# Optimization experiments

Measured on AMD Instinct MI355X. Metric: run time of the kernel, lower is better.

Reference implementation:

```python
import jax, jax.numpy as jnp
import numpy as np

B, T, C, H, HS = 4, 2048, 384, 6, 64
EPS = 1e-5


def setup_inputs() -> dict:
    key = jax.random.key(0)
    ks = jax.random.split(key, 8)
    s = lambda fan_in: 1.0 / np.sqrt(fan_in)
    return {
        "x": jax.random.normal(ks[0], (B, T, C), jnp.float32),
        "wq": jax.random.normal(ks[1], (H, C, HS), jnp.float32) * s(C),
        "wk": jax.random.normal(ks[2], (H, C, HS), jnp.float32) * s(C),
        "wv": jax.random.normal(ks[3], (H, C, HS), jnp.float32) * s(C),
        "w_proj": jax.random.normal(ks[4], (C, C), jnp.float32) * s(C),
        "b_proj": jnp.zeros((C,), jnp.float32),
        "w1": jax.random.normal(ks[5], (C, 4 * C), jnp.float32) * s(C),
        "b1": jnp.zeros((4 * C,), jnp.float32),
        "w2": jax.random.normal(ks[6], (4 * C, C), jnp.float32) * s(4 * C),
        "b2": jnp.zeros((C,), jnp.float32),
        "g1": jnp.ones((C,), jnp.float32),
        "be1": jnp.zeros((C,), jnp.float32),
        "g2": jnp.ones((C,), jnp.float32),
        "be2": jnp.zeros((C,), jnp.float32),
    }


def _layernorm(z, g, b):
    m = jnp.mean(z, axis=-1, keepdims=True)
    v = jnp.mean((z - m) ** 2, axis=-1, keepdims=True)
    return (z - m) * jax.lax.rsqrt(v + EPS) * g + b


def reference(x, wq, wk, wv, w_proj, b_proj, w1, b1, w2, b2, g1, be1, g2, be2):
    Bx, Tx, Cx = x.shape
    h = _layernorm(x, g1, be1)
    # per-head projections, no bias
    q = jnp.einsum('btc,hcd->bhtd', h, wq)
    k = jnp.einsum('btc,hcd->bhtd', h, wk)
    v = jnp.einsum('btc,hcd->bhtd', h, wv)
    # NOTE: source scales by full embedding dim C, not head_size
    scores = jnp.einsum('bhtd,bhsd->bhts', q, k) * (Cx ** -0.5)
    mask = jnp.tril(jnp.ones((Tx, Tx), bool))  # tril causal mask
    scores = jnp.where(mask[None, None], scores, -jnp.inf)
    # Faithful to source: softmax over dim=1 of (B,T,T) == QUERY axis (axis=2 here)
    w = jax.nn.softmax(scores, axis=2)
    out = jnp.einsum('bhts,bhsd->bhtd', w, v)
    out = out.transpose(0, 2, 1, 3).reshape(Bx, Tx, Cx)  # concat heads
    out = out @ w_proj + b_proj
    x = x + out  # residual 1
    h2 = _layernorm(x, g2, be2)
    f = jax.nn.relu(h2 @ w1 + b1) @ w2 + b2
    return x + f  # residual 2
```

## Files before the change

kernel.cpp:

```cpp
#include <hip/hip_runtime.h>
#include <hip/hip_bf16.h>


#define BB 4
#define TT 2048
#define CC 384
#define HH 6
#define HS 64
#define BT 8192
#define C4 1536
#define VST 2080
#define SCALE 0.05103103630798288f

typedef __attribute__((ext_vector_type(8))) short short8;
typedef __attribute__((ext_vector_type(4))) float f32x4;
typedef __hip_bfloat16 bf16_t;

__device__ inline short8 ld8(const bf16_t* p) { return *reinterpret_cast<const short8*>(p); }
__device__ inline float tof(float v) { return v; }
__device__ inline float tof(bf16_t v) { return __bfloat162float(v); }
#define MFMA(a, b, c) __builtin_amdgcn_mfma_f32_16x16x32_bf16(a, b, c, 0, 0, 0)

__global__ __launch_bounds__(256) void zinit_kernel(float* __restrict__ p, int n4) {
    int i = blockIdx.x * 256 + threadIdx.x;
    if (i < n4) ((f32x4*)p)[i] = (f32x4){0.f, 0.f, 0.f, 0.f};
}

__global__ __launch_bounds__(256) void castbf_kernel(const float* __restrict__ src,
                                                     bf16_t* __restrict__ dst) {
    int i = (blockIdx.x * 256 + threadIdx.x) * 4;
    f32x4 v = *(const f32x4*)(src + i);
#pragma unroll
    for (int j = 0; j < 4; j++) dst[i + j] = __float2bfloat16(v[j]);
}

__device__ inline void tc(const float* __restrict__ src, bf16_t* __restrict__ dst,
                          int R, int Cc, int idx) {
    int rc = R * Cc;
    int b = idx / rc;
    int rem = idx - b * rc;
    int c = rem / R;
    int r = rem - c * R;
    dst[b * rc + c * R + r] = __float2bfloat16(src[b * rc + r * Cc + c]);
}
#define RW  147456
#define RW1 589824
#define NTC (3*RW + RW + 2*RW1)
#define NZ  (BT*CC/4)
__global__ __launch_bounds__(256) void prep_kernel(const float* __restrict__ wq,
                                                   const float* __restrict__ wk,
                                                   const float* __restrict__ wv,
                                                   const float* __restrict__ wproj,
                                                   const float* __restrict__ w1,
                                                   const float* __restrict__ w2,
                                                   bf16_t* __restrict__ wall,
                                                   bf16_t* __restrict__ wpt,
                                                   bf16_t* __restrict__ w1t,
                                                   bf16_t* __restrict__ w2t,
                                                   float* __restrict__ attnf) {
    int i = blockIdx.x * 256 + threadIdx.x;
    if (i < RW)                tc(wq, wall, CC, HS, i);
    else if (i < 2*RW)         tc(wk, wall + RW, CC, HS, i - RW);
    else if (i < 3*RW)         tc(wv, wall + 2*RW, CC, HS, i - 2*RW);
    else if (i < 4*RW)         tc(wproj, wpt, CC, CC, i - 3*RW);
    else if (i < 4*RW + RW1)   tc(w1, w1t, CC, C4, i - 4*RW);
    else if (i < NTC)          tc(w2, w2t, C4, CC, i - 4*RW - RW1);
    else {
        int z = i - NTC;
        if (z < NZ) ((f32x4*)attnf)[z] = (f32x4){0.f, 0.f, 0.f, 0.f};
    }
}

template <typename T>
__global__ __launch_bounds__(256) void ln_kernel(const T* __restrict__ x,
                                                 const float* __restrict__ g,
                                                 const float* __restrict__ be,
                                                 bf16_t* __restrict__ out) {
    int wave = threadIdx.x >> 6, lane = threadIdx.x & 63;
    int row = blockIdx.x * 4 + wave;
    const T* xr = x + (size_t)row * CC;
    float v[6];
    float s = 0.f;
#pragma unroll
    for (int i = 0; i < 6; i++) { v[i] = tof(xr[lane + i * 64]); s += v[i]; }
#pragma unroll
    for (int off = 32; off > 0; off >>= 1) s += __shfl_xor(s, off, 64);
    float mean = s * (1.f / 384.f);
    float s2 = 0.f;
#pragma unroll
    for (int i = 0; i < 6; i++) { float d = v[i] - mean; s2 += d * d; }
#pragma unroll
    for (int off = 32; off > 0; off >>= 1) s2 += __shfl_xor(s2, off, 64);
    float rstd = rsqrtf(s2 * (1.f / 384.f) + 1e-5f);
    bf16_t* orow = out + (size_t)row * CC;
#pragma unroll
    for (int i = 0; i < 6; i++) {
        int c = lane + i * 64;
        orow[c] = __float2bfloat16((v[i] - mean) * rstd * g[c] + be[c]);
    }
}

template <int KDIM, int EPI>
__global__ __launch_bounds__(256) void gemm128_kernel(const bf16_t* __restrict__ A,
                                                      const bf16_t* __restrict__ Bt,
                                                      const float* __restrict__ bias,
                                                      const void* __restrict__ resid,
                                                      void* __restrict__ o0,
                                                      void* __restrict__ o1,
                                                      void* __restrict__ o2, int N) {
    const int m0 = blockIdx.x * 128, n0 = blockIdx.y * 128;
    const int tid = threadIdx.x;
    const int lane = tid & 63, wave = tid >> 6;
    const int r16 = lane & 15, quad = lane >> 4;
    const int wm = (wave >> 1) * 64, wn = (wave & 1) * 64;
    __shared__ bf16_t Ash[128][40];
    __shared__ bf16_t Bsh[128][40];
    f32x4 zero = {0.f, 0.f, 0.f, 0.f};
    f32x4 acc[4][4];
#pragma unroll
    for (int i = 0; i < 4; i++)
#pragma unroll
        for (int j = 0; j < 4; j++) acc[i][j] = zero;
    const int srow = tid >> 2;
    const int scol = (tid & 3) * 8;
    for (int k0 = 0; k0 < KDIM; k0 += 32) {
        const bf16_t* Ag = A + (size_t)(m0 + srow) * KDIM + k0 + scol;
        const bf16_t* Bg = Bt + (size_t)(n0 + srow) * KDIM + k0 + scol;
        short8 a0 = ld8(Ag);
        short8 a1 = ld8(Ag + (size_t)64 * KDIM);
        short8 b0 = ld8(Bg);
        short8 b1 = ld8(Bg + (size_t)64 * KDIM);
        *(short8*)&Ash[srow][scol]      = a0;
        *(short8*)&Ash[64 + srow][scol] = a1;
        *(short8*)&Bsh[srow][scol]      = b0;
        *(short8*)&Bsh[64 + srow][scol] = b1;
        __syncthreads();
        short8 af[4], bfr[4];
#pragma unroll
        for (int i = 0; i < 4; i++) af[i]  = *(const short8*)&Ash[wm + i * 16 + r16][quad * 8];
#pragma unroll
        for (int i = 0; i < 4; i++) bfr[i] = *(const short8*)&Bsh[wn + i * 16 + r16][quad * 8];
#pragma unroll
        for (int mi = 0; mi < 4; mi++)
#pragma unroll
            for (int ni = 0; ni < 4; ni++)
                acc[mi][ni] = MFMA(af[mi], bfr[ni], acc[mi][ni]);
        __syncthreads();
    }
#pragma unroll
    for (int mi = 0; mi < 4; mi++)
#pragma unroll
        for (int ni = 0; ni < 4; ni++)
#pragma unroll
            for (int reg = 0; reg < 4; reg++) {
                int m = m0 + wm + mi * 16 + quad * 4 + reg;
                int n = n0 + wn + ni * 16 + r16;
                float val = acc[mi][ni][reg];
                if constexpr (EPI == 0) {
                    val += bias[n] + ((const float*)resid)[(size_t)m * N + n];
                    ((bf16_t*)o0)[(size_t)m * N + n] = __float2bfloat16(val);
                } else if constexpr (EPI == 1) {
                    val = fmaxf(val + bias[n], 0.f);
                    ((bf16_t*)o0)[(size_t)m * N + n] = __float2bfloat16(val);
                } else if constexpr (EPI == 2) {
                    val += bias[n] + tof(((const bf16_t*)resid)[(size_t)m * N + n]);
                    ((float*)o0)[(size_t)m * N + n] = val;
                } else {
                    int mat = n / 384;
                    int nr  = n - mat * 384;
                    int head = nr >> 6, d = nr & 63;
                    int b = m >> 11, t = m & 2047;
                    int bh = b * HH + head;
                    bf16_t bv = __float2bfloat16(val);
                    if (mat == 0)      ((bf16_t*)o0)[(size_t)(bh * TT + t) * HS + d] = bv;
                    else if (mat == 1) ((bf16_t*)o1)[(size_t)(bh * TT + t) * HS + d] = bv;
                    else               ((bf16_t*)o2)[(size_t)(bh * HS + d) * VST + t] = bv;
                }
            }
}

__global__ __launch_bounds__(256) void colsum_kernel(const bf16_t* __restrict__ qbf,
                                                     const bf16_t* __restrict__ kbf,
                                                     float* __restrict__ colsum) {
    int stile = blockIdx.x, bh = blockIdx.y, z = blockIdx.z;
    if (stile + z * 8 > 31) return;
    int s0 = stile * 64;
    const int lane = threadIdx.x & 63, wave = threadIdx.x >> 6;
    const int r16 = lane & 15, quad = lane >> 4;
    __shared__ bf16_t Ksh[64][72];
    __shared__ float csum[64];
    if (threadIdx.x < 64) csum[threadIdx.x] = 0.f;
    {
        const int srow = threadIdx.x >> 2, scol = (threadIdx.x & 3) << 4;
        const bf16_t* kp = kbf + (size_t)(bh * TT + s0 + srow) * HS + scol;
        *(short8*)&Ksh[srow][scol]     = ld8(kp);
        *(short8*)&Ksh[srow][scol + 8] = ld8(kp + 8);
    }
    __syncthreads();
    short8 bfr[4][2];
#pragma unroll
    for (int ns = 0; ns < 4; ns++)
#pragma unroll
        for (int kk = 0; kk < 2; kk++)
            bfr[ns][kk] = *(const short8*)&Ksh[ns * 16 + r16][kk * 32 + quad * 8];
    float colacc[4] = {0.f, 0.f, 0.f, 0.f};
    for (int jj = wave; jj < 8; jj += 4) {
        int tt = stile + z * 8 + jj;
        if (tt > 31) break;
#pragma unroll
        for (int ms = 0; ms < 4; ms++) {
            const bf16_t* qp = qbf + (size_t)(bh * TT + tt * 64 + ms * 16 + r16) * HS + quad * 8;
            short8 a0 = ld8(qp);
            short8 a1 = ld8(qp + 32);
#pragma unroll
            for (int ns = 0; ns < 4; ns++) {
                f32x4 sacc = {0.f, 0.f, 0.f, 0.f};
                sacc = MFMA(a0, bfr[ns][0], sacc);
                sacc = MFMA(a1, bfr[ns][1], sacc);
#pragma unroll
                for (int reg = 0; reg < 4; reg++) {
                    int t = tt * 64 + ms * 16 + quad * 4 + reg;
                    int s = s0 + ns * 16 + r16;
                    if (s <= t) colacc[ns] += __expf(sacc[reg] * SCALE);
                }
            }
        }
    }
#pragma unroll
    for (int ns = 0; ns < 4; ns++) atomicAdd(&csum[ns * 16 + r16], colacc[ns]);
    __syncthreads();
    if (threadIdx.x < 64) atomicAdd(&colsum[bh * TT + s0 + threadIdx.x], csum[threadIdx.x]);
}

__global__ __launch_bounds__(256) void attn_part_kernel(const bf16_t* __restrict__ qbf,
                                                        const bf16_t* __restrict__ kbf,
                                                        const bf16_t* __restrict__ vst,
                                                        const float* __restrict__ colsum,
                                                        float* __restrict__ attnf) {
    int ttile = blockIdx.x, bh = blockIdx.y, z = blockIdx.z;
    int sbeg = z * 8;
    if (sbeg > ttile) return;
    int send = ttile + 1 < sbeg + 8 ? ttile + 1 : sbeg + 8;
    int t0 = ttile * 64;
    const int lane = threadIdx.x & 63, wave = threadIdx.x >> 6;
    const int r16 = lane & 15, quad = lane >> 4;
    __shared__ bf16_t Ksh[64][72];
    __shared__ bf16_t Vsh[64][72];
    __shared__ bf16_t El[64][72];
    __shared__ float Crc[64];
    const int srow = threadIdx.x >> 2;
    const int scol = (threadIdx.x & 3) << 4;
    f32x4 zero = {0.f, 0.f, 0.f, 0.f};
    f32x4 oacc[4] = {zero, zero, zero, zero};
    const bf16_t* qp = qbf + (size_t)(bh * TT + t0 + wave * 16 + r16) * HS + quad * 8;
    short8 qa0 = ld8(qp);
    short8 qa1 = ld8(qp + 32);
    for (int st = sbeg; st < send; st++) {
        int s0 = st * 64;
        {
            const bf16_t* kp = kbf + (size_t)(bh * TT + s0 + srow) * HS + scol;
            short8 k0 = ld8(kp);
            short8 k1 = ld8(kp + 8);
            const bf16_t* vp = vst + (size_t)(bh * HS + srow) * VST + s0 + scol;
            short8 v0 = ld8(vp);
            short8 v1 = ld8(vp + 8);
            *(short8*)&Ksh[srow][scol]     = k0;
            *(short8*)&Ksh[srow][scol + 8] = k1;
            *(short8*)&Vsh[srow][scol]     = v0;
            *(short8*)&Vsh[srow][scol + 8] = v1;
            if (threadIdx.x < 64)
                Crc[threadIdx.x] = 1.0f / colsum[bh * TT + s0 + threadIdx.x];
        }
        __syncthreads();
#pragma unroll
        for (int ns = 0; ns < 4; ns++) {
            float rc = Crc[ns * 16 + r16];
            f32x4 sacc = zero;
            sacc = MFMA(qa0, *(const short8*)&Ksh[ns * 16 + r16][quad * 8], sacc);
            sacc = MFMA(qa1, *(const short8*)&Ksh[ns * 16 + r16][32 + quad * 8], sacc);
#pragma unroll
            for (int reg = 0; reg < 4; reg++) {
                int t = t0 + wave * 16 + quad * 4 + reg;
                int s = s0 + ns * 16 + r16;
                float e = (s <= t) ? __expf(sacc[reg] * SCALE) * rc : 0.f;
                El[wave * 16 + quad * 4 + reg][ns * 16 + r16] = __float2bfloat16(e);
            }
        }
#pragma unroll
        for (int ks = 0; ks < 2; ks++) {
            short8 ea = ld8(&El[wave * 16 + r16][ks * 32 + quad * 8]);
#pragma unroll
            for (int ns = 0; ns < 4; ns++) {
                short8 vb = *(const short8*)&Vsh[ns * 16 + r16][ks * 32 + quad * 8];
                oacc[ns] = MFMA(ea, vb, oacc[ns]);
            }
        }
        __syncthreads();
    }
    int b = bh / HH, head = bh - b * HH;
#pragma unroll
    for (int ns = 0; ns < 4; ns++)
#pragma unroll
        for (int reg = 0; reg < 4; reg++) {
            int t = t0 + wave * 16 + quad * 4 + reg;
            int d = ns * 16 + r16;
            atomicAdd(&attnf[(size_t)(b * TT + t) * CC + head * HS + d], oacc[ns][reg]);
        }
}

extern "C" void kernel_launch(void* const* d_in, const int* in_sizes, int n_in,
                              void* d_out, int out_size, void* d_ws, size_t ws_size,
                              hipStream_t stream) {
    const float* x      = (const float*)d_in[0];
    const float* wq     = (const float*)d_in[1];
    const float* wk     = (const float*)d_in[2];
    const float* wv     = (const float*)d_in[3];
    const float* w_proj = (const float*)d_in[4];
    const float* b_proj = (const float*)d_in[5];
    const float* w1     = (const float*)d_in[6];
    const float* b1     = (const float*)d_in[7];
    const float* w2     = (const float*)d_in[8];
    const float* b2     = (const float*)d_in[9];
    const float* g1     = (const float*)d_in[10];
    const float* be1    = (const float*)d_in[11];
    const float* g2     = (const float*)d_in[12];
    const float* be2    = (const float*)d_in[13];
    float* out = (float*)d_out;

    char* p = (char*)d_ws;
    auto alloc = [&](size_t bytes) {
        void* r = (void*)p;
        p += (bytes + 255) & ~(size_t)255;
        return r;
    };
    const size_t ACT  = (size_t)BT * CC * 2;
    bf16_t* wqt    = (bf16_t*)alloc(HH * HS * CC * 2);
    bf16_t* wkt    = (bf16_t*)alloc(HH * HS * CC * 2);
    bf16_t* wvt    = (bf16_t*)alloc(HH * HS * CC * 2);
    bf16_t* wpt    = (bf16_t*)alloc(CC * CC * 2);
    bf16_t* w1t    = (bf16_t*)alloc((size_t)C4 * CC * 2);
    bf16_t* w2t    = (bf16_t*)alloc((size_t)CC * C4 * 2);
    char* slotA = (char*)alloc(ACT);
    char* slotB = (char*)alloc(2 * ACT);
    char* slotC = (char*)alloc((size_t)24 * HS * VST * 2);

    bf16_t* h_bf    = (bf16_t*)slotA;
    bf16_t* attn_bf = (bf16_t*)slotA;
    bf16_t* h2_bf   = (bf16_t*)slotA;
    bf16_t* q_bf    = (bf16_t*)slotB;
    bf16_t* k_bf    = (bf16_t*)(slotB + ACT);
    bf16_t* f1      = (bf16_t*)slotB;
    bf16_t* v_bf    = (bf16_t*)slotC;
    bf16_t* x1b     = (bf16_t*)slotC;
    float* colsum   = (float*)wqt;
    float* attn_f   = (float*)d_out;
    (void)wkt; (void)wvt;

    prep_kernel<<<(NTC + NZ + 255) / 256, 256, 0, stream>>>(
        wq, wk, wv, w_proj, w1, w2, wqt, wpt, w1t, w2t, attn_f);
    ln_kernel<float><<<BT/4, 256, 0, stream>>>(x, g1, be1, h_bf);
    gemm128_kernel<CC, 3><<<dim3(BT/128, 9), 256, 0, stream>>>(
        h_bf, wqt, nullptr, nullptr, q_bf, k_bf, v_bf, 1152);
    zinit_kernel<<<48, 256, 0, stream>>>(colsum, 24*TT/4);
    colsum_kernel<<<dim3(32, 24, 4), 256, 0, stream>>>(q_bf, k_bf, colsum);
    attn_part_kernel<<<dim3(32, 24, 4), 256, 0, stream>>>(q_bf, k_bf, v_bf, colsum, attn_f);
    castbf_kernel<<<3072, 256, 0, stream>>>(attn_f, attn_bf);
    gemm128_kernel<CC, 0><<<dim3(BT/128, CC/128), 256, 0, stream>>>(
        attn_bf, wpt, b_proj, x, x1b, nullptr, nullptr, CC);
    ln_kernel<bf16_t><<<BT/4, 256, 0, stream>>>(x1b, g2, be2, h2_bf);
    for (int c = 0; c < 2; c++) {
        size_t m0 = (size_t)c * 4096;
        gemm128_kernel<CC, 1><<<dim3(4096/128, C4/128), 256, 0, stream>>>(
            h2_bf + m0 * CC, w1t, b1, nullptr, f1, nullptr, nullptr, C4);
        gemm128_kernel<C4, 2><<<dim3(4096/128, CC/128), 256, 0, stream>>>(
            f1, w2t, b2, x1b + m0 * CC, out + m0 * CC, nullptr, nullptr, CC);
    }
}
```

Measured before the change: 343.4 us.

## Pair causal query tiles per block and write bf16 attention output directly

Replaces the split-K attention pass, which spread each query tile over up to four source chunks and merged them with fp32 atomics, with one block per pair of query tiles (i and 31-i) that walks the full causal range. Each block does the same amount of work, so the load stays balanced, and the result goes straight to bf16 without atomics. This removes the zero-init of the fp32 buffer, the atomicAdd traffic and the separate cast kernel. In exchange, only 384 blocks run each serial loop over 33 key tiles, which cuts parallelism and may underfill the GPU's compute units.

```diff
diff --git a/kernel.cpp b/kernel.cpp
--- a/kernel.cpp
+++ b/kernel.cpp
@@ -26,14 +26,6 @@
     if (i < n4) ((f32x4*)p)[i] = (f32x4){0.f, 0.f, 0.f, 0.f};
 }
 
-__global__ __launch_bounds__(256) void castbf_kernel(const float* __restrict__ src,
-                                                     bf16_t* __restrict__ dst) {
-    int i = (blockIdx.x * 256 + threadIdx.x) * 4;
-    f32x4 v = *(const f32x4*)(src + i);
-#pragma unroll
-    for (int j = 0; j < 4; j++) dst[i + j] = __float2bfloat16(v[j]);
-}
-
 __device__ inline void tc(const float* __restrict__ src, bf16_t* __restrict__ dst,
                           int R, int Cc, int idx) {
     int rc = R * Cc;
@@ -46,7 +38,6 @@
 #define RW  147456
 #define RW1 589824
 #define NTC (3*RW + RW + 2*RW1)
-#define NZ  (BT*CC/4)
 __global__ __launch_bounds__(256) void prep_kernel(const float* __restrict__ wq,
                                                    const float* __restrict__ wk,
                                                    const float* __restrict__ wv,
@@ -56,8 +47,7 @@
                                                    bf16_t* __restrict__ wall,
                                                    bf16_t* __restrict__ wpt,
                                                    bf16_t* __restrict__ w1t,
-                                                   bf16_t* __restrict__ w2t,
-                                                   float* __restrict__ attnf) {
+                                                   bf16_t* __restrict__ w2t) {
     int i = blockIdx.x * 256 + threadIdx.x;
     if (i < RW)                tc(wq, wall, CC, HS, i);
     else if (i < 2*RW)         tc(wk, wall + RW, CC, HS, i - RW);
@@ -65,10 +55,6 @@
     else if (i < 4*RW)         tc(wproj, wpt, CC, CC, i - 3*RW);
     else if (i < 4*RW + RW1)   tc(w1, w1t, CC, C4, i - 4*RW);
     else if (i < NTC)          tc(w2, w2t, C4, CC, i - 4*RW - RW1);
-    else {
-        int z = i - NTC;
-        if (z < NZ) ((f32x4*)attnf)[z] = (f32x4){0.f, 0.f, 0.f, 0.f};
-    }
 }
 
 template <typename T>
@@ -232,16 +218,12 @@
     if (threadIdx.x < 64) atomicAdd(&colsum[bh * TT + s0 + threadIdx.x], csum[threadIdx.x]);
 }
 
-__global__ __launch_bounds__(256) void attn_part_kernel(const bf16_t* __restrict__ qbf,
+__global__ __launch_bounds__(256) void attn_pair_kernel(const bf16_t* __restrict__ qbf,
                                                         const bf16_t* __restrict__ kbf,
                                                         const bf16_t* __restrict__ vst,
                                                         const float* __restrict__ colsum,
-                                                        float* __restrict__ attnf) {
-    int ttile = blockIdx.x, bh = blockIdx.y, z = blockIdx.z;
-    int sbeg = z * 8;
-    if (sbeg > ttile) return;
-    int send = ttile + 1 < sbeg + 8 ? ttile + 1 : sbeg + 8;
-    int t0 = ttile * 64;
+                                                        bf16_t* __restrict__ attnb) {
+    int bh = blockIdx.y;
     const int lane = threadIdx.x & 63, wave = threadIdx.x >> 6;
     const int r16 = lane & 15, quad = lane >> 4;
     __shared__ bf16_t Ksh[64][72];
@@ -251,61 +233,65 @@
     const int srow = threadIdx.x >> 2;
     const int scol = (threadIdx.x & 3) << 4;
     f32x4 zero = {0.f, 0.f, 0.f, 0.f};
-    f32x4 oacc[4] = {zero, zero, zero, zero};
-    const bf16_t* qp = qbf + (size_t)(bh * TT + t0 + wave * 16 + r16) * HS + quad * 8;
-    short8 qa0 = ld8(qp);
-    short8 qa1 = ld8(qp + 32);
-    for (int st = sbeg; st < send; st++) {
-        int s0 = st * 64;
-        {
-            const bf16_t* kp = kbf + (size_t)(bh * TT + s0 + srow) * HS + scol;
-            short8 k0 = ld8(kp);
-            short8 k1 = ld8(kp + 8);
-            const bf16_t* vp = vst + (size_t)(bh * HS + srow) * VST + s0 + scol;
-            short8 v0 = ld8(vp);
-            short8 v1 = ld8(vp + 8);
-            *(short8*)&Ksh[srow][scol]     = k0;
-            *(short8*)&Ksh[srow][scol + 8] = k1;
-            *(short8*)&Vsh[srow][scol]     = v0;
-            *(short8*)&Vsh[srow][scol + 8] = v1;
-            if (threadIdx.x < 64)
-                Crc[threadIdx.x] = 1.0f / colsum[bh * TT + s0 + threadIdx.x];
+    int b = bh / HH, head = bh - b * HH;
+    for (int half = 0; half < 2; half++) {
+        int ttile = half ? 31 - blockIdx.x : blockIdx.x;
+        int t0 = ttile * 64;
+        f32x4 oacc[4] = {zero, zero, zero, zero};
+        const bf16_t* qp = qbf + (size_t)(bh * TT + t0 + wave * 16 + r16) * HS + quad * 8;
+        short8 qa0 = ld8(qp);
+        short8 qa1 = ld8(qp + 32);
+        for (int st = 0; st <= ttile; st++) {
+            int s0 = st * 64;
+            {
+                const bf16_t* kp = kbf + (size_t)(bh * TT + s0 + srow) * HS + scol;
+                short8 k0 = ld8(kp);
+                short8 k1 = ld8(kp + 8);
+                const bf16_t* vp = vst + (size_t)(bh * HS + srow) * VST + s0 + scol;
+                short8 v0 = ld8(vp);
+                short8 v1 = ld8(vp + 8);
+                *(short8*)&Ksh[srow][scol]     = k0;
+                *(short8*)&Ksh[srow][scol + 8] = k1;
+                *(short8*)&Vsh[srow][scol]     = v0;
+                *(short8*)&Vsh[srow][scol + 8] = v1;
+                if (threadIdx.x < 64)
+                    Crc[threadIdx.x] = 1.0f / colsum[bh * TT + s0 + threadIdx.x];
+            }
+            __syncthreads();
+#pragma unroll
+            for (int ns = 0; ns < 4; ns++) {
+                float rc = Crc[ns * 16 + r16];
+                f32x4 sacc = zero;
+                sacc = MFMA(qa0, *(const short8*)&Ksh[ns * 16 + r16][quad * 8], sacc);
+                sacc = MFMA(qa1, *(const short8*)&Ksh[ns * 16 + r16][32 + quad * 8], sacc);
+#pragma unroll
+                for (int reg = 0; reg < 4; reg++) {
+                    int t = t0 + wave * 16 + quad * 4 + reg;
+                    int s = s0 + ns * 16 + r16;
+                    float e = (s <= t) ? __expf(sacc[reg] * SCALE) * rc : 0.f;
+                    El[wave * 16 + quad * 4 + reg][ns * 16 + r16] = __float2bfloat16(e);
+                }
+            }
+#pragma unroll
+            for (int ks = 0; ks < 2; ks++) {
+                short8 ea = ld8(&El[wave * 16 + r16][ks * 32 + quad * 8]);
+#pragma unroll
+                for (int ns = 0; ns < 4; ns++) {
+                    short8 vb = *(const short8*)&Vsh[ns * 16 + r16][ks * 32 + quad * 8];
+                    oacc[ns] = MFMA(ea, vb, oacc[ns]);
+                }
+            }
+            __syncthreads();
         }
-        __syncthreads();
-#pragma unroll
-        for (int ns = 0; ns < 4; ns++) {
-            float rc = Crc[ns * 16 + r16];
-            f32x4 sacc = zero;
-            sacc = MFMA(qa0, *(const short8*)&Ksh[ns * 16 + r16][quad * 8], sacc);
-            sacc = MFMA(qa1, *(const short8*)&Ksh[ns * 16 + r16][32 + quad * 8], sacc);
+#pragma unroll
+        for (int ns = 0; ns < 4; ns++)
 #pragma unroll
             for (int reg = 0; reg < 4; reg++) {
                 int t = t0 + wave * 16 + quad * 4 + reg;
-                int s = s0 + ns * 16 + r16;
-                float e = (s <= t) ? __expf(sacc[reg] * SCALE) * rc : 0.f;
-                El[wave * 16 + quad * 4 + reg][ns * 16 + r16] = __float2bfloat16(e);
-            }
-        }
-#pragma unroll
-        for (int ks = 0; ks < 2; ks++) {
-            short8 ea = ld8(&El[wave * 16 + r16][ks * 32 + quad * 8]);
-#pragma unroll
-            for (int ns = 0; ns < 4; ns++) {
-                short8 vb = *(const short8*)&Vsh[ns * 16 + r16][ks * 32 + quad * 8];
-                oacc[ns] = MFMA(ea, vb, oacc[ns]);
-            }
-        }
-        __syncthreads();
-    }
-    int b = bh / HH, head = bh - b * HH;
-#pragma unroll
-    for (int ns = 0; ns < 4; ns++)
-#pragma unroll
-        for (int reg = 0; reg < 4; reg++) {
-            int t = t0 + wave * 16 + quad * 4 + reg;
-            int d = ns * 16 + r16;
-            atomicAdd(&attnf[(size_t)(b * TT + t) * CC + head * HS + d], oacc[ns][reg]);
-        }
+                int d = ns * 16 + r16;
+                attnb[(size_t)(b * TT + t) * CC + head * HS + d] = __float2bfloat16(oacc[ns][reg]);
+            }
+    }
 }
 
 extern "C" void kernel_launch(void* const* d_in, const int* in_sizes, int n_in,
@@ -353,18 +339,16 @@
     bf16_t* v_bf    = (bf16_t*)slotC;
     bf16_t* x1b     = (bf16_t*)slotC;
     float* colsum   = (float*)wqt;
-    float* attn_f   = (float*)d_out;
     (void)wkt; (void)wvt;
 
-    prep_kernel<<<(NTC + NZ + 255) / 256, 256, 0, stream>>>(
-        wq, wk, wv, w_proj, w1, w2, wqt, wpt, w1t, w2t, attn_f);
+    prep_kernel<<<(NTC + 255) / 256, 256, 0, stream>>>(
+        wq, wk, wv, w_proj, w1, w2, wqt, wpt, w1t, w2t);
     ln_kernel<float><<<BT/4, 256, 0, stream>>>(x, g1, be1, h_bf);
     gemm128_kernel<CC, 3><<<dim3(BT/128, 9), 256, 0, stream>>>(
         h_bf, wqt, nullptr, nullptr, q_bf, k_bf, v_bf, 1152);
     zinit_kernel<<<48, 256, 0, stream>>>(colsum, 24*TT/4);
     colsum_kernel<<<dim3(32, 24, 4), 256, 0, stream>>>(q_bf, k_bf, colsum);
-    attn_part_kernel<<<dim3(32, 24, 4), 256, 0, stream>>>(q_bf, k_bf, v_bf, colsum, attn_f);
-    castbf_kernel<<<3072, 256, 0, stream>>>(attn_f, attn_bf);
+    attn_pair_kernel<<<dim3(16, 24), 256, 0, stream>>>(q_bf, k_bf, v_bf, colsum, attn_bf);
     gemm128_kernel<CC, 0><<<dim3(BT/128, CC/128), 256, 0, stream>>>(
         attn_bf, wpt, b_proj, x, x1b, nullptr, nullptr, CC);
     ln_kernel<bf16_t><<<BT/4, 256, 0, stream>>>(x1b, g2, be2, h2_bf);
```

After: 345.7 us. Within noise of the previous version (+0.7%).
